# Optimization experiments

Hardware: AMD Instinct MI355X
Metric: run time of the kernel (lower is better)

Reference implementation:

```python
import jax, jax.numpy as jnp
import numpy as np

B, IN, H, OUT = 4096, 1024, 1024, 1024


def setup_inputs() -> dict:
    key = jax.random.key(0)
    ks = jax.random.split(key, 16)
    s_in = 1.0 / np.sqrt(IN)
    s_h = 1.0 / np.sqrt(H)
    d = {}
    d['input_vec'] = jax.random.normal(ks[0], (B, IN), jnp.float32)
    d['hidden_vec'] = jax.random.normal(ks[1], (B, H), jnp.float32)
    d['cell_vec'] = jax.random.normal(ks[2], (B, H), jnp.float32)
    names = ['f', 'i', 'o', 'g']
    for j, n in enumerate(names):
        d['Wx_' + n] = jax.random.uniform(ks[3 + 3 * j], (H, IN), jnp.float32, -s_in, s_in)
        d['bx_' + n] = jax.random.uniform(ks[4 + 3 * j], (H,), jnp.float32, -s_in, s_in)
        d['Wh_' + n] = jax.random.uniform(ks[5 + 3 * j], (H, H), jnp.float32, -s_h, s_h)
    d['W_out'] = jax.random.uniform(ks[15], (OUT, H), jnp.float32, -s_h, s_h)
    d['b_out'] = jax.random.uniform(jax.random.fold_in(key, 99), (OUT,), jnp.float32, -s_h, s_h)
    return d


def reference(input_vec, hidden_vec, cell_vec,
              Wx_f, bx_f, Wh_f,
              Wx_i, bx_i, Wh_i,
              Wx_o, bx_o, Wh_o,
              Wx_g, bx_g, Wh_g,
              W_out, b_out):
    # Fuse the 8 small linears into two GEMMs: [B,IN]x[IN,4H] and [B,H]x[H,4H].
    Wx = jnp.concatenate([Wx_f, Wx_i, Wx_o, Wx_g], axis=0)   # [4H, IN]
    Wh = jnp.concatenate([Wh_f, Wh_i, Wh_o, Wh_g], axis=0)   # [4H, H]
    b = jnp.concatenate([bx_f, bx_i, bx_o, bx_g], axis=0)    # [4H]
    gates = input_vec @ Wx.T + hidden_vec @ Wh.T + b          # [B, 4H]
    f, i, o, g = jnp.split(gates, 4, axis=1)
    f = jax.nn.sigmoid(f)
    i = jax.nn.sigmoid(i)
    o = jax.nn.sigmoid(o)
    g = jnp.tanh(g)
    new_cell = f * cell_vec + i * g
    new_hidden = o * jnp.tanh(new_cell)
    output_vec = new_hidden @ W_out.T + b_out
    return (new_hidden, new_cell, output_vec)
```

## Files before the change

### kernel.cpp

```cpp
#include <hip/hip_runtime.h>
#include <hip/hip_bf16.h>
#include <stdint.h>

#define B_   4096
#define IN_  1024
#define H_   1024
#define OUT_ 1024

typedef __attribute__((ext_vector_type(8)))  short short8;
typedef __attribute__((ext_vector_type(16))) float floatx16;

__device__ static inline void gload_lds16(const void* g, void* l) {
    __builtin_amdgcn_global_load_lds(
        (const __attribute__((address_space(1))) unsigned int*)g,
        (__attribute__((address_space(3))) unsigned int*)l,
        16, 0, 0);
}

__device__ static inline float sigmoidf_(float x) { return 1.0f / (1.0f + __expf(-x)); }
__device__ static inline float tanhf_(float x)    { return 1.0f - 2.0f / (1.0f + __expf(2.0f * x)); }

struct Ptrs8 { const float* p[8]; };

__global__ __launch_bounds__(256) void cvt_all_kernel(
        const float* __restrict__ x, const float* __restrict__ h,
        Ptrs8 ptrs, const float* __restrict__ wout,
        __hip_bfloat16* __restrict__ xh,
        __hip_bfloat16* __restrict__ Wc,
        __hip_bfloat16* __restrict__ Wob) {
    const int nth = gridDim.x * blockDim.x;
    for (int g = blockIdx.x * blockDim.x + threadIdx.x; g < 2228224; g += nth) {
        const float* src;
        __hip_bfloat16* dst;
        if (g < 1048576) {
            int b  = g >> 8;
            int c8 = (g & 255) * 8;
            src = (c8 < IN_) ? (x + (size_t)b * IN_ + c8)
                             : (h + (size_t)b * H_ + (c8 - IN_));
            dst = xh + (size_t)b * 2048 + c8;
        } else if (g < 2097152) {
            int gg = g - 1048576;
            int n  = gg >> 8;
            int c8 = (gg & 255) * 8;
            int gate = (n >> 5) & 3;
            int hh   = ((n >> 7) << 5) + (n & 31);
            src = (c8 < 1024) ? (ptrs.p[2 * gate]     + (size_t)hh * 1024 + c8)
                              : (ptrs.p[2 * gate + 1] + (size_t)hh * 1024 + (c8 - 1024));
            dst = Wc + (size_t)n * 2048 + c8;
        } else {
            int gg = g - 2097152;
            src = wout + (size_t)gg * 8;
            dst = Wob + (size_t)gg * 8;
        }
        float4 v0 = *(const float4*)src;
        float4 v1 = *(const float4*)(src + 4);
        __hip_bfloat16 tmp[8];
        tmp[0] = __float2bfloat16(v0.x);
        tmp[1] = __float2bfloat16(v0.y);
        tmp[2] = __float2bfloat16(v0.z);
        tmp[3] = __float2bfloat16(v0.w);
        tmp[4] = __float2bfloat16(v1.x);
        tmp[5] = __float2bfloat16(v1.y);
        tmp[6] = __float2bfloat16(v1.z);
        tmp[7] = __float2bfloat16(v1.w);
        *(uint4*)dst = *(const uint4*)tmp;
    }
}

__global__ __launch_bounds__(512, 2) void gemm_gate_fused(
    const __hip_bfloat16* __restrict__ A,
    const __hip_bfloat16* __restrict__ Bm,
    const float* __restrict__ cell,
    const float* __restrict__ bxf, const float* __restrict__ bxi,
    const float* __restrict__ bxo, const float* __restrict__ bxg,
    float* __restrict__ new_hidden, float* __restrict__ new_cell,
    __hip_bfloat16* __restrict__ hb)
{
    constexpr int K = 2048;

    __shared__ short sA0[16384];
    __shared__ short sB0[16384];
    __shared__ short sA1[16384];
    __shared__ short sB1[16384];

    const int tid  = threadIdx.x;
    const int lane = tid & 63;
    const int wv   = tid >> 6;
    const int wr   = wv >> 1;
    const int wc   = wv & 1;

    const int bid    = blockIdx.x;
    const int xcd    = bid & 7;
    const int loc    = bid >> 3;
    const int n_tile = xcd * 2 + (loc & 1);
    const int m_tile = loc >> 1;
    const int m0 = m_tile * 256;
    const int n0 = n_tile * 256;

    const int srow   = tid >> 3;
    const int schunk = tid & 7;
    const int scg    = schunk ^ (srow & 7);
    const __hip_bfloat16* Ag = A  + (size_t)(m0 + srow) * K + scg * 8;
    const __hip_bfloat16* Bg = Bm + (size_t)(n0 + srow) * K + scg * 8;
    const int wvoff = wv * 1024;

    const int fr    = lane & 31;
    const int khalf = lane >> 5;
    const int sw    = fr & 7;

    int offA[2], offB[4];
    #pragma unroll
    for (int i = 0; i < 2; ++i) offA[i] = (wr * 64 + i * 32 + fr) * 128;
    #pragma unroll
    for (int j = 0; j < 4; ++j) offB[j] = (wc * 128 + j * 32 + fr) * 128;

    floatx16 acc[2][4] = {};

    #pragma unroll
    for (int s = 0; s < 4; ++s)
        gload_lds16(Ag + (size_t)(s * 64) * K, (char*)sA0 + s * 8192 + wvoff);
    #pragma unroll
    for (int s = 0; s < 4; ++s)
        gload_lds16(Bg + (size_t)(s * 64) * K, (char*)sB0 + s * 8192 + wvoff);

#define TILE_BODY(RA, RB, WA, WB, tnext, DO_STAGE)                                        \
    {                                                                                     \
                         \
        __builtin_amdgcn_s_barrier();                                                     \
        if (DO_STAGE) {                                                                   \
            const __hip_bfloat16* Agt = Ag + (size_t)(tnext) * 64;                        \
            const __hip_bfloat16* Bgt = Bg + (size_t)(tnext) * 64;                        \
            _Pragma("unroll")                                                             \
            for (int s = 0; s < 4; ++s)                                                   \
                gload_lds16(Agt + (size_t)(s * 64) * K, (char*)(WA) + s * 8192 + wvoff);  \
            _Pragma("unroll")                                                             \
            for (int s = 0; s < 4; ++s)                                                   \
                gload_lds16(Bgt + (size_t)(s * 64) * K, (char*)(WB) + s * 8192 + wvoff);  \
                   \
            asm volatile("s_waitcnt vmcnt(8)" ::: "memory");                              \
        } else {                                                                          \
            asm volatile("s_waitcnt vmcnt(0)" ::: "memory");                              \
        }                                                                                 \
                              \
        __builtin_amdgcn_s_barrier();                                                     \
        __builtin_amdgcn_sched_barrier(0);                                                \
             \
        _Pragma("unroll")                                                                 \
        for (int kk = 0; kk < 4; ++kk) {                                                  \
            const int co = ((kk * 2 + khalf) ^ sw) * 16;                                  \
            short8 af[2], bfr[4];                                                         \
            _Pragma("unroll")                                                             \
            for (int i = 0; i < 2; ++i)                                                   \
                af[i]  = *(const short8*)((const char*)(RA) + offA[i] + co);              \
            _Pragma("unroll")                                                             \
            for (int j = 0; j < 4; ++j)                                                   \
                bfr[j] = *(const short8*)((const char*)(RB) + offB[j] + co);              \
            __builtin_amdgcn_s_setprio(1);                                                \
            _Pragma("unroll")                                                             \
            for (int i = 0; i < 2; ++i)                                                   \
                _Pragma("unroll")                                                         \
                for (int j = 0; j < 4; ++j)                                               \
                    acc[i][j] = __builtin_amdgcn_mfma_f32_32x32x16_bf16(                  \
                        af[i], bfr[j], acc[i][j], 0, 0, 0);                               \
            __builtin_amdgcn_s_setprio(0);                                                \
        }                                                                                 \
    }

    #pragma unroll 1
    for (int t2 = 0; t2 < 16; ++t2) {
        TILE_BODY(sA0, sB0, sA1, sB1, 2 * t2 + 1, true);
        TILE_BODY(sA1, sB1, sA0, sB0, 2 * t2 + 2, (t2 < 15));
    }
#undef TILE_BODY

    const int h  = ((n0 + wc * 128) >> 2) + fr;
    const float bfb = bxf[h];
    const float bib = bxi[h];
    const float bob = bxo[h];
    const float bgb = bxg[h];

    #pragma unroll
    for (int i = 0; i < 2; ++i) {
        const int row_base = m0 + wr * 64 + i * 32 + 4 * khalf;
        #pragma unroll
        for (int reg = 0; reg < 16; ++reg) {
            const int row = row_base + (reg & 3) + 8 * (reg >> 2);
            const size_t off = (size_t)row * H_ + h;
            const float f  = sigmoidf_(acc[i][0][reg] + bfb);
            const float ii = sigmoidf_(acc[i][1][reg] + bib);
            const float o  = sigmoidf_(acc[i][2][reg] + bob);
            const float g  = tanhf_(acc[i][3][reg] + bgb);
            const float c  = f * cell[off] + ii * g;
            const float nh = o * tanhf_(c);
            new_cell[off]   = c;
            new_hidden[off] = nh;
            hb[off] = __float2bfloat16(nh);
        }
    }
}

__global__ __launch_bounds__(256, 2) void gemm_out(
    const __hip_bfloat16* __restrict__ A,
    const __hip_bfloat16* __restrict__ Bm,
    float* __restrict__ C,
    const float* __restrict__ bias)
{
    constexpr int K  = 1024;
    constexpr int N  = 1024;

    __shared__ short oA0[8192];
    __shared__ short oB0[4096];
    __shared__ short oA1[8192];
    __shared__ short oB1[4096];

    const int tid  = threadIdx.x;
    const int lane = tid & 63;
    const int wv   = tid >> 6;

    const int bid    = blockIdx.x;
    const int xcd    = bid & 7;
    const int loc    = bid >> 3;
    const int n_tile = xcd * 2 + (loc & 1);
    const int m_tile = loc >> 1;
    const int m0 = m_tile * 128;
    const int n0 = n_tile * 64;

    const int srow   = tid >> 3;
    const int schunk = tid & 7;
    const int scg    = schunk ^ (srow & 7);
    const __hip_bfloat16* Ag = A  + (size_t)(m0 + srow) * K + scg * 8;
    const __hip_bfloat16* Bg = Bm + (size_t)(n0 + srow) * K + scg * 8;
    const int wvoff = wv * 1024;

    const int wrow  = wv * 32;
    const int fr    = lane & 31;
    const int khalf = lane >> 5;
    const int sw    = fr & 7;

    const int offA = (wrow + fr) * 128;
    int offB[2];
    #pragma unroll
    for (int j = 0; j < 2; ++j) offB[j] = (j * 32 + fr) * 128;
    const int swA = (wrow + fr) & 7;

    floatx16 acc[2] = {};

    #pragma unroll
    for (int s = 0; s < 4; ++s)
        gload_lds16(Ag + (size_t)(s * 32) * K, (char*)oA0 + s * 4096 + wvoff);
    #pragma unroll
    for (int s = 0; s < 2; ++s)
        gload_lds16(Bg + (size_t)(s * 32) * K, (char*)oB0 + s * 4096 + wvoff);

#define OTILE_BODY(RA, RB, WA, WB, k_next, DO_STAGE)                                      \
    {                                                                                     \
        __builtin_amdgcn_s_barrier();                                                     \
        if (DO_STAGE) {                                                                   \
            _Pragma("unroll")                                                             \
            for (int s = 0; s < 4; ++s)                                                   \
                gload_lds16(Ag + (size_t)(s * 32) * K + (k_next),                         \
                            (char*)(WA) + s * 4096 + wvoff);                              \
            _Pragma("unroll")                                                             \
            for (int s = 0; s < 2; ++s)                                                   \
                gload_lds16(Bg + (size_t)(s * 32) * K + (k_next),                         \
                            (char*)(WB) + s * 4096 + wvoff);                              \
            asm volatile("s_waitcnt vmcnt(6)" ::: "memory");                              \
        } else {                                                                          \
            asm volatile("s_waitcnt vmcnt(0)" ::: "memory");                              \
        }                                                                                 \
        __builtin_amdgcn_s_barrier();                                                     \
        __builtin_amdgcn_sched_barrier(0);                                                \
        _Pragma("unroll")                                                                 \
        for (int kk = 0; kk < 4; ++kk) {                                                  \
            const int cg = kk * 2 + khalf;                                                \
            short8 af = *(const short8*)((const char*)(RA) + offA + ((cg ^ swA) * 16));   \
            short8 bf[2];                                                                 \
            _Pragma("unroll")                                                             \
            for (int j = 0; j < 2; ++j)                                                   \
                bf[j] = *(const short8*)((const char*)(RB) + offB[j] + ((cg ^ sw) * 16)); \
            __builtin_amdgcn_s_setprio(1);                                                \
            _Pragma("unroll")                                                             \
            for (int j = 0; j < 2; ++j)                                                   \
                acc[j] = __builtin_amdgcn_mfma_f32_32x32x16_bf16(af, bf[j], acc[j], 0, 0, 0); \
            __builtin_amdgcn_s_setprio(0);                                                \
        }                                                                                 \
    }

    #pragma unroll 1
    for (int t2 = 0; t2 < 8; ++t2) {
        OTILE_BODY(oA0, oB0, oA1, oB1, (2 * t2 + 1) * 64, true);
        OTILE_BODY(oA1, oB1, oA0, oB0, (2 * t2 + 2) * 64, (t2 < 7));
    }
#undef OTILE_BODY

    #pragma unroll
    for (int j = 0; j < 2; ++j) {
        const int col = n0 + j * 32 + fr;
        const float bb = bias[col];
        #pragma unroll
        for (int reg = 0; reg < 16; ++reg) {
            const int row = m0 + wrow + 4 * khalf + (reg & 3) + 8 * (reg >> 2);
            C[(size_t)row * N + col] = acc[j][reg] + bb;
        }
    }
}

extern "C" void kernel_launch(void* const* d_in, const int* in_sizes, int n_in,
                              void* d_out, int out_size, void* d_ws, size_t ws_size,
                              hipStream_t stream) {
    const float* input_vec  = (const float*)d_in[0];
    const float* hidden_vec = (const float*)d_in[1];
    const float* cell_vec   = (const float*)d_in[2];
    const float* Wx_f = (const float*)d_in[3];
    const float* bx_f = (const float*)d_in[4];
    const float* Wh_f = (const float*)d_in[5];
    const float* Wx_i = (const float*)d_in[6];
    const float* bx_i = (const float*)d_in[7];
    const float* Wh_i = (const float*)d_in[8];
    const float* Wx_o = (const float*)d_in[9];
    const float* bx_o = (const float*)d_in[10];
    const float* Wh_o = (const float*)d_in[11];
    const float* Wx_g = (const float*)d_in[12];
    const float* bx_g = (const float*)d_in[13];
    const float* Wh_g = (const float*)d_in[14];
    const float* W_out = (const float*)d_in[15];
    const float* b_out = (const float*)d_in[16];

    char* ws = (char*)d_ws;
    __hip_bfloat16* xh  = (__hip_bfloat16*)(ws);
    __hip_bfloat16* Wc  = (__hip_bfloat16*)(ws + (16ull << 20));
    __hip_bfloat16* Wob = (__hip_bfloat16*)(ws + (32ull << 20));
    __hip_bfloat16* hb  = (__hip_bfloat16*)(ws + (34ull << 20));

    float* new_hidden = (float*)d_out;
    float* new_cell   = new_hidden + (size_t)B_ * H_;
    float* out_vec    = new_cell + (size_t)B_ * H_;

    Ptrs8 p;
    p.p[0] = Wx_f; p.p[1] = Wh_f; p.p[2] = Wx_i; p.p[3] = Wh_i;
    p.p[4] = Wx_o; p.p[5] = Wh_o; p.p[6] = Wx_g; p.p[7] = Wh_g;
    cvt_all_kernel<<<2048, 256, 0, stream>>>(input_vec, hidden_vec, p, W_out, xh, Wc, Wob);

    gemm_gate_fused<<<256, 512, 0, stream>>>(
        xh, Wc, cell_vec, bx_f, bx_i, bx_o, bx_g, new_hidden, new_cell, hb);

    gemm_out<<<512, 256, 0, stream>>>(hb, Wob, out_vec, b_out);
}
```

Baseline: 240.8 us.

## Rework gate GEMM with 16x16 MFMA, 2x4 wave layout and interleaved half-tile staging

Rewrites the fused gate GEMM main loop to use 16x16x32 bf16 MFMA on a 2x4 wave grid, with each wave owning a 128x64 sub-tile. LDS is split into half-tile buffers, and global-to-LDS staging is interleaved at quarter-tile granularity between MFMA groups, so loads overlap compute more finely. The weight interleave in the convert kernel changes from 32-row to 16-row gate groups to match the new epilogue column mapping. This adds many more barriers per iteration and more accumulator registers, which could hurt occupancy at 512 threads with 2 blocks per CU.

```diff
diff --git a/kernel.cpp b/kernel.cpp
--- a/kernel.cpp
+++ b/kernel.cpp
@@ -8,6 +8,7 @@
 #define OUT_ 1024
 
 typedef __attribute__((ext_vector_type(8)))  short short8;
+typedef __attribute__((ext_vector_type(4)))  float floatx4;
 typedef __attribute__((ext_vector_type(16))) float floatx16;
 
 __device__ static inline void gload_lds16(const void* g, void* l) {
@@ -42,8 +43,8 @@
             int gg = g - 1048576;
             int n  = gg >> 8;
             int c8 = (gg & 255) * 8;
-            int gate = (n >> 5) & 3;
-            int hh   = ((n >> 7) << 5) + (n & 31);
+            int gate = (n >> 4) & 3;
+            int hh   = ((n >> 6) << 4) + (n & 15);
             src = (c8 < 1024) ? (ptrs.p[2 * gate]     + (size_t)hh * 1024 + c8)
                               : (ptrs.p[2 * gate + 1] + (size_t)hh * 1024 + (c8 - 1024));
             dst = Wc + (size_t)n * 2048 + c8;
@@ -78,16 +79,20 @@
 {
     constexpr int K = 2048;
 
-    __shared__ short sA0[16384];
-    __shared__ short sB0[16384];
-    __shared__ short sA1[16384];
-    __shared__ short sB1[16384];
+    __shared__ short A0h0[8192];
+    __shared__ short A0h1[8192];
+    __shared__ short B0h0[8192];
+    __shared__ short B0h1[8192];
+    __shared__ short A1h0[8192];
+    __shared__ short A1h1[8192];
+    __shared__ short B1h0[8192];
+    __shared__ short B1h1[8192];
 
     const int tid  = threadIdx.x;
     const int lane = tid & 63;
     const int wv   = tid >> 6;
-    const int wr   = wv >> 1;
-    const int wc   = wv & 1;
+    const int wm   = wv >> 2;
+    const int wn   = wv & 3;
 
     const int bid    = blockIdx.x;
     const int xcd    = bid & 7;
@@ -98,98 +103,123 @@
     const int n0 = n_tile * 256;
 
     const int srow   = tid >> 3;
-    const int schunk = tid & 7;
-    const int scg    = schunk ^ (srow & 7);
+    const int scg    = (tid & 7) ^ (srow & 7);
     const __hip_bfloat16* Ag = A  + (size_t)(m0 + srow) * K + scg * 8;
     const __hip_bfloat16* Bg = Bm + (size_t)(n0 + srow) * K + scg * 8;
     const int wvoff = wv * 1024;
 
-    const int fr    = lane & 31;
-    const int khalf = lane >> 5;
-    const int sw    = fr & 7;
-
-    int offA[2], offB[4];
-    #pragma unroll
-    for (int i = 0; i < 2; ++i) offA[i] = (wr * 64 + i * 32 + fr) * 128;
-    #pragma unroll
-    for (int j = 0; j < 4; ++j) offB[j] = (wc * 128 + j * 32 + fr) * 128;
-
-    floatx16 acc[2][4] = {};
-
-    #pragma unroll
-    for (int s = 0; s < 4; ++s)
-        gload_lds16(Ag + (size_t)(s * 64) * K, (char*)sA0 + s * 8192 + wvoff);
-    #pragma unroll
-    for (int s = 0; s < 4; ++s)
-        gload_lds16(Bg + (size_t)(s * 64) * K, (char*)sB0 + s * 8192 + wvoff);
-
-#define TILE_BODY(RA, RB, WA, WB, tnext, DO_STAGE)                                        \
-    {                                                                                     \
-                         \
-        __builtin_amdgcn_s_barrier();                                                     \
-        if (DO_STAGE) {                                                                   \
-            const __hip_bfloat16* Agt = Ag + (size_t)(tnext) * 64;                        \
-            const __hip_bfloat16* Bgt = Bg + (size_t)(tnext) * 64;                        \
-            _Pragma("unroll")                                                             \
-            for (int s = 0; s < 4; ++s)                                                   \
-                gload_lds16(Agt + (size_t)(s * 64) * K, (char*)(WA) + s * 8192 + wvoff);  \
-            _Pragma("unroll")                                                             \
-            for (int s = 0; s < 4; ++s)                                                   \
-                gload_lds16(Bgt + (size_t)(s * 64) * K, (char*)(WB) + s * 8192 + wvoff);  \
-                   \
-            asm volatile("s_waitcnt vmcnt(8)" ::: "memory");                              \
-        } else {                                                                          \
-            asm volatile("s_waitcnt vmcnt(0)" ::: "memory");                              \
-        }                                                                                 \
-                              \
-        __builtin_amdgcn_s_barrier();                                                     \
-        __builtin_amdgcn_sched_barrier(0);                                                \
-             \
-        _Pragma("unroll")                                                                 \
-        for (int kk = 0; kk < 4; ++kk) {                                                  \
-            const int co = ((kk * 2 + khalf) ^ sw) * 16;                                  \
-            short8 af[2], bfr[4];                                                         \
-            _Pragma("unroll")                                                             \
-            for (int i = 0; i < 2; ++i)                                                   \
-                af[i]  = *(const short8*)((const char*)(RA) + offA[i] + co);              \
-            _Pragma("unroll")                                                             \
-            for (int j = 0; j < 4; ++j)                                                   \
-                bfr[j] = *(const short8*)((const char*)(RB) + offB[j] + co);              \
-            __builtin_amdgcn_s_setprio(1);                                                \
-            _Pragma("unroll")                                                             \
-            for (int i = 0; i < 2; ++i)                                                   \
-                _Pragma("unroll")                                                         \
-                for (int j = 0; j < 4; ++j)                                               \
-                    acc[i][j] = __builtin_amdgcn_mfma_f32_32x32x16_bf16(                  \
-                        af[i], bfr[j], acc[i][j], 0, 0, 0);                               \
-            __builtin_amdgcn_s_setprio(0);                                                \
-        }                                                                                 \
-    }
+    const int fr16 = lane & 15;
+    const int q    = lane >> 4;
+    const int frb  = fr16 * 128;
+    const int bb   = (wn & 1) * 8192;
+    int ck[2];
+    #pragma unroll
+    for (int ks = 0; ks < 2; ++ks) ck[ks] = (((ks * 4 + q) ^ (lane & 7)) << 4);
+
+    const short* myA0 = wm ? A0h1 : A0h0;
+    const short* myA1 = wm ? A1h1 : A1h0;
+    const short* myB0 = (wn >> 1) ? B0h1 : B0h0;
+    const short* myB1 = (wn >> 1) ? B1h1 : B1h0;
+
+    short8  fA[4][2];
+    short8  fB[4][2];
+    floatx4 acc[8][4] = {};
+
+#define STG_A(DST, hh, t) do {                                                            \
+    gload_lds16(Ag + (size_t)((hh)*128 +  0) * K + (size_t)(t) * 64,                      \
+                (char*)(DST) + 0 * 8192 + wvoff);                                         \
+    gload_lds16(Ag + (size_t)((hh)*128 + 64) * K + (size_t)(t) * 64,                      \
+                (char*)(DST) + 1 * 8192 + wvoff);                                         \
+} while (0)
+#define STG_B(DST, hh, t) do {                                                            \
+    gload_lds16(Bg + (size_t)((hh)*128 +  0) * K + (size_t)(t) * 64,                      \
+                (char*)(DST) + 0 * 8192 + wvoff);                                         \
+    gload_lds16(Bg + (size_t)((hh)*128 + 64) * K + (size_t)(t) * 64,                      \
+                (char*)(DST) + 1 * 8192 + wvoff);                                         \
+} while (0)
+#define READ_A(ARR, mh) do {                                                              \
+    _Pragma("unroll") for (int i = 0; i < 4; ++i)                                         \
+    _Pragma("unroll") for (int ks = 0; ks < 2; ++ks)                                      \
+        fA[i][ks] = *(const short8*)((const char*)(ARR) + (mh)*8192 + i*2048 + frb + ck[ks]); \
+} while (0)
+#define READ_B(ARR, nh) do {                                                              \
+    _Pragma("unroll") for (int jj = 0; jj < 2; ++jj)                                      \
+    _Pragma("unroll") for (int ks = 0; ks < 2; ++ks)                                      \
+        fB[(nh)*2+jj][ks] = *(const short8*)((const char*)(ARR) + bb + ((nh)*2+jj)*2048 + frb + ck[ks]); \
+} while (0)
+#define MFMA_Q(mh, nh) do {                                                               \
+    __builtin_amdgcn_s_setprio(1);                                                        \
+    _Pragma("unroll") for (int i = 0; i < 4; ++i)                                         \
+    _Pragma("unroll") for (int jj = 0; jj < 2; ++jj)                                      \
+    _Pragma("unroll") for (int ks = 0; ks < 2; ++ks)                                      \
+        acc[(mh)*4+i][(nh)*2+jj] = __builtin_amdgcn_mfma_f32_16x16x32_bf16(               \
+            fA[i][ks], fB[(nh)*2+jj][ks], acc[(mh)*4+i][(nh)*2+jj], 0, 0, 0);             \
+    __builtin_amdgcn_s_setprio(0);                                                        \
+} while (0)
+#define BAR __builtin_amdgcn_s_barrier()
+#define VM4 asm volatile("s_waitcnt vmcnt(4)" ::: "memory")
+
+    STG_B(B0h0, 0, 0); STG_B(B0h1, 1, 0);
+    STG_A(A0h0, 0, 0); STG_A(A0h1, 1, 0);
+    STG_B(B1h0, 0, 1); STG_A(A1h0, 0, 1);
+    VM4;
+    BAR;
 
     #pragma unroll 1
-    for (int t2 = 0; t2 < 16; ++t2) {
-        TILE_BODY(sA0, sB0, sA1, sB1, 2 * t2 + 1, true);
-        TILE_BODY(sA1, sB1, sA0, sB0, 2 * t2 + 2, (t2 < 15));
-    }
-#undef TILE_BODY
-
-    const int h  = ((n0 + wc * 128) >> 2) + fr;
-    const float bfb = bxf[h];
-    const float bib = bxi[h];
-    const float bob = bxo[h];
-    const float bgb = bxg[h];
-
-    #pragma unroll
-    for (int i = 0; i < 2; ++i) {
-        const int row_base = m0 + wr * 64 + i * 32 + 4 * khalf;
+    for (int it = 0; it < 16; ++it) {
+        const int t1 = 2 * it + 1;
+        const int t2 = 2 * it + 2;
+        const int t3 = 2 * it + 3;
+
+        READ_A(myA0, 0); READ_B(myB0, 0);
+        STG_B(B1h1, 1, t1);
+        BAR; MFMA_Q(0, 0); BAR;
+        READ_B(myB0, 1);
+        STG_A(A1h1, 1, t1);
+        BAR; MFMA_Q(0, 1); BAR;
+        READ_A(myA0, 1);
+        STG_B(B0h0, 0, t2);
+        BAR; MFMA_Q(1, 0); BAR;
+        STG_B(B0h1, 1, t2);
+        BAR; MFMA_Q(1, 1); VM4; BAR;
+        READ_A(myA1, 0); READ_B(myB1, 0);
+        STG_A(A0h0, 0, t2);
+        BAR; MFMA_Q(0, 0); BAR;
+        READ_B(myB1, 1);
+        STG_A(A0h1, 1, t2);
+        BAR; MFMA_Q(0, 1); BAR;
+        READ_A(myA1, 1);
+        STG_B(B1h0, 0, t3);
+        BAR; MFMA_Q(1, 0); BAR;
+        STG_A(A1h0, 0, t3);
+        BAR; MFMA_Q(1, 1); VM4; BAR;
+    }
+
+#undef STG_A
+#undef STG_B
+#undef READ_A
+#undef READ_B
+#undef MFMA_Q
+#undef BAR
+#undef VM4
+
+    const int hcol = ((n0 + wn * 64) >> 2) + fr16;
+    const float bfb = bxf[hcol];
+    const float bib = bxi[hcol];
+    const float bob = bxo[hcol];
+    const float bgb = bxg[hcol];
+
+    #pragma unroll
+    for (int m = 0; m < 8; ++m) {
+        const int row_base = m0 + wm * 128 + m * 16 + q * 4;
         #pragma unroll
-        for (int reg = 0; reg < 16; ++reg) {
-            const int row = row_base + (reg & 3) + 8 * (reg >> 2);
-            const size_t off = (size_t)row * H_ + h;
-            const float f  = sigmoidf_(acc[i][0][reg] + bfb);
-            const float ii = sigmoidf_(acc[i][1][reg] + bib);
-            const float o  = sigmoidf_(acc[i][2][reg] + bob);
-            const float g  = tanhf_(acc[i][3][reg] + bgb);
+        for (int reg = 0; reg < 4; ++reg) {
+            const int row = row_base + reg;
+            const size_t off = (size_t)row * H_ + hcol;
+            const float f  = sigmoidf_(acc[m][0][reg] + bfb);
+            const float ii = sigmoidf_(acc[m][1][reg] + bib);
+            const float o  = sigmoidf_(acc[m][2][reg] + bob);
+            const float g  = tanhf_(acc[m][3][reg] + bgb);
             const float c  = f * cell[off] + ii * g;
             const float nh = o * tanhf_(c);
             new_cell[off]   = c;
```

Result: faster. 234.2 us, median of 2 (-2.7%).
